# Kernel optimization log

Measured on AMD Instinct MI355X. Metric: run time of the kernel, lower is better.

Reference implementation:

```python
import jax, jax.numpy as jnp
import numpy as np

B, C, T, K = 64, 12, 2048, 2048
LMAX = 11            # max kernel length among {7,9,11}
CMAX = C - 1         # torch.randint(1, C) -> at most C-1 selected channels
PL = 1024            # left pad: covers max 'same' left pad = (dil*(len-1))//2 <= (T-1)//2
PR = 3412            # right pad: covers zero-weight padded taps (LMAX-1)*dil_max
A = 7.0              # softppv_param


def setup_inputs() -> dict:
    rng = np.random.default_rng(0)
    klens = rng.choice(np.array([7, 9, 11]), size=K)
    nch = rng.integers(1, C, size=K)  # 1..C-1 channels per kernel
    weights = np.zeros((K, CMAX, LMAX), np.float32)
    ch_idx = np.zeros((K, CMAX), np.int32)
    dils = np.zeros(K, np.int32)
    offs = np.zeros(K, np.int32)
    olens = np.zeros(K, np.int32)
    for k in range(K):
        n, L = int(nch[k]), int(klens[k])
        ch_idx[k, :n] = rng.permutation(C)[:n]
        w = rng.standard_normal((n, L)).astype(np.float32)
        w -= w.mean(axis=1, keepdims=True)  # per-channel mean-centering as in torch init
        weights[k, :n, :L] = w
        d = int(2.0 ** rng.uniform(0.0, np.log2((T - 1) / (L - 1))))
        dils[k] = d
        if rng.integers(0, 2) == 0:  # padding='same' (torch: left=total//2, right=rest)
            offs[k] = PL - (d * (L - 1)) // 2
            olens[k] = T
        else:                        # padding='valid'
            offs[k] = PL
            olens[k] = T - d * (L - 1)
    biases = rng.uniform(0.0, 1.0, size=K).astype(np.float32)
    x = jax.random.normal(jax.random.key(0), (B, C, T), jnp.float32)
    return {
        "x": x,
        "weights": jnp.asarray(weights),
        "biases": jnp.asarray(biases),
        "ch_idx": jnp.asarray(ch_idx),
        "dils": jnp.asarray(dils),
        "offs": jnp.asarray(offs),
        "olens": jnp.asarray(olens),
    }


def reference(x, weights, biases, ch_idx, dils, offs, olens):
    # x: (B, C, T). Zero-pad time axis once so every (same/valid, dilation) variant
    # becomes a pure gather with a per-kernel offset; zero-padded weight taps/channels
    # contribute nothing, so padded gathers are harmless.
    xpad = jnp.pad(x, ((0, 0), (0, 0), (PL, PR)))
    t = jnp.arange(T)
    l = jnp.arange(LMAX)

    def step(_, p):
        W, b, ch, d, off, olen = p
        pos = off + t[:, None] + l[None, :] * d            # (T, LMAX) tap positions
        Xg = xpad[:, ch, :][:, :, pos]                     # (B, CMAX, T, LMAX)
        y = jnp.einsum('bctl,cl->bt', Xg, W) + b           # cross-correlation + bias
        mask = t < olen                                    # valid output positions
        ppv = jnp.sum(jax.nn.sigmoid(A * y - 3.0) * mask, axis=-1) / olen
        mx = jnp.max(jnp.where(mask, y, -jnp.inf), axis=-1)
        return None, (ppv, mx)

    _, (ppvs, mxs) = jax.lax.scan(step, None, (weights, biases, ch_idx, dils, offs, olens))
    # torch concatenates [ppv_k, max_k] per kernel along the feature axis -> (B, 2K)
    return jnp.stack([ppvs.T, mxs.T], axis=-1).reshape(x.shape[0], 2 * K)
```

## Files before the change

kernel.cpp:

```cpp
#include <hip/hip_runtime.h>
#include <math.h>

#define B_SZ   64
#define C_SZ   12
#define T_SZ   2048
#define K_SZ   2048
#define LMAX   11
#define CMAX   11
#define NPAIR  6
#define PL_PAD 1024
#define A_PARAM 7.0f

#define NW     8
#define BLOCK_MAIN (NW * 64)
#define R      16
#define SPL    4
#define NBLK   768

typedef _Float16 h2 __attribute__((ext_vector_type(2)));

__device__ __forceinline__ float fdot2f(unsigned w, unsigned v, float acc) {
    return __builtin_amdgcn_fdot2(__builtin_bit_cast(h2, w),
                                  __builtin_bit_cast(h2, v), acc, false);
}

__global__ __launch_bounds__(256) void trh_kernel(const float* __restrict__ x,
                                                  unsigned short* __restrict__ xT) {
    const int c    = blockIdx.x;
    const int lane = threadIdx.x & 63;
    const int wid  = threadIdx.x >> 6;
    const int t0   = blockIdx.y * 128 + wid * 32;
    const float* xrow = x + ((size_t)lane * C_SZ + c) * T_SZ + t0;
    unsigned short* dst = xT + ((size_t)c * T_SZ + t0) * 64 + lane;
    #pragma unroll 8
    for (int i = 0; i < 32; ++i) {
        const _Float16 h = (_Float16)xrow[i];
        dst[i * 64] = __builtin_bit_cast(unsigned short, h);
    }
}

__global__ __launch_bounds__(1024) void sched_kernel(const float* __restrict__ w,
                                                     const int* __restrict__ olens,
                                                     unsigned* __restrict__ perm,
                                                     unsigned* __restrict__ meta,
                                                     unsigned* __restrict__ counter) {
    __shared__ unsigned key[K_SZ];
    const int tid = threadIdx.x;
    if (tid == 0) *counter = 0u;

    for (int k = tid; k < K_SZ; k += 1024) {
        const float* wk = w + (size_t)k * (CMAX * LMAX);
        int n = 0, L = 0;
        for (int e = 0; e < CMAX * LMAX; ++e) {
            if (wk[e] != 0.0f) {
                const int c = e / LMAX, l = e % LMAX;
                n = max(n, c + 1);
                L = max(L, l + 1);
            }
        }
        meta[k] = (unsigned)n | ((unsigned)L << 8);
        const unsigned cost = (unsigned)(n * L) * (unsigned)((olens[k] + 127) >> 7);
        key[k] = (cost << 11) | (unsigned)k;
    }
    __syncthreads();

    for (int ksz = 2; ksz <= K_SZ; ksz <<= 1) {
        for (int j = ksz >> 1; j > 0; j >>= 1) {
            for (int i = tid; i < K_SZ; i += 1024) {
                const int ixj = i ^ j;
                if (ixj > i) {
                    const unsigned a = key[i], b = key[ixj];
                    const bool sw = ((i & ksz) == 0) ? (a < b) : (a > b);
                    if (sw) { key[i] = b; key[ixj] = a; }
                }
            }
            __syncthreads();
        }
    }
    for (int i = tid; i < K_SZ; i += 1024)
        perm[i] = key[i] & 0x7FFu;
}

template<int LC>
__device__ __forceinline__ void conv_all(
    const unsigned short* __restrict__ xT,
    const int*      __restrict__ sCh,
    const unsigned  (* __restrict__ sWp)[LMAX],
    int npair, int d, int offr, int olen, float bias, int sp,
    int lane, int wid, float& psum, float& pmax)
{
    constexpr int NV = R + LC - 1;

    const int nj   = (olen + d - 1) / d;
    const int njb  = (nj + R - 1) / R;
    const int S    = (d >= 64) ? 1 : ((64 + d - 1) / d);
    const int len  = (njb + S - 1) / S;
    const int nunits = d * S;

    for (int u = sp * NW + wid; u < nunits; u += NW * SPL) {
        int q, seg;
        if (S == 1) { q = u; seg = 0; }
        else        { q = u % d; seg = u / d; }
        const int jb0 = seg * len;
        const int jb1 = min(njb, jb0 + len);

        for (int jb = jb0; jb < jb1; ++jb) {
            const int tq = q + jb * (R * d);
            if (tq >= olen) break;
            const int tpos0 = tq + offr;

            float y[R];
            #pragma unroll
            for (int r = 0; r < R; ++r) y[r] = bias;

            const bool fast = (tpos0 >= 0) && (tpos0 + (NV - 1) * d < T_SZ);

            if (fast) {
                for (int p = 0; p < npair; ++p) {
                    const int rbA = __builtin_amdgcn_readfirstlane(sCh[2*p  ] * T_SZ + tpos0);
                    const int rbB = __builtin_amdgcn_readfirstlane(sCh[2*p+1] * T_SZ + tpos0);
                    const unsigned short* rpA = xT + ((size_t)rbA << 6);
                    const unsigned short* rpB = xT + ((size_t)rbB << 6);

                    unsigned vp[NV];
                    #pragma unroll
                    for (int i = 0; i < NV; ++i) {
                        const unsigned a = rpA[lane];
                        const unsigned b = rpB[lane];
                        vp[i] = __builtin_amdgcn_perm(b, a, 0x05040100);
                        rpA += (d << 6); rpB += (d << 6);
                    }

                    const unsigned* wrow = &sWp[p][0];
                    #pragma unroll
                    for (int l = 0; l < LC; ++l) {
                        const unsigned w = wrow[l];
                        #pragma unroll
                        for (int r = 0; r < R; ++r)
                            y[r] = fdot2f(w, vp[l + r], y[r]);
                    }
                }
            } else {
                for (int p = 0; p < npair; ++p) {
                    const int rbA = __builtin_amdgcn_readfirstlane(sCh[2*p  ] * T_SZ);
                    const int rbB = __builtin_amdgcn_readfirstlane(sCh[2*p+1] * T_SZ);
                    const unsigned short* rowA = xT + ((size_t)rbA << 6);
                    const unsigned short* rowB = xT + ((size_t)rbB << 6);

                    unsigned vp[NV];
                    #pragma unroll
                    for (int i = 0; i < NV; ++i) {
                        const int tp  = tpos0 + i * d;
                        const int tpc = min(max(tp, 0), T_SZ - 1);
                        const unsigned a = rowA[((size_t)tpc << 6) + lane];
                        const unsigned b = rowB[((size_t)tpc << 6) + lane];
                        const unsigned pk = __builtin_amdgcn_perm(b, a, 0x05040100);
                        vp[i] = ((unsigned)tp < (unsigned)T_SZ) ? pk : 0u;
                    }

                    const unsigned* wrow = &sWp[p][0];
                    #pragma unroll
                    for (int l = 0; l < LC; ++l) {
                        const unsigned w = wrow[l];
                        #pragma unroll
                        for (int r = 0; r < R; ++r)
                            y[r] = fdot2f(w, vp[l + r], y[r]);
                    }
                }
            }

            #pragma unroll
            for (int r = 0; r < R; ++r) {
                const int t = tq + r * d;
                if (t < olen) {
                    psum += 1.0f / (1.0f + __expf(3.0f - A_PARAM * y[r]));
                    pmax  = fmaxf(pmax, y[r]);
                }
            }
        }
    }
}

__global__ __launch_bounds__(BLOCK_MAIN, 3) void rocket_tr(
    const unsigned short* __restrict__ xT,
    const unsigned* __restrict__ perm,
    const unsigned* __restrict__ meta,
    const float* __restrict__ weights,
    const float* __restrict__ biases,
    const int*   __restrict__ ch_idx,
    const int*   __restrict__ dils,
    const int*   __restrict__ offs,
    const int*   __restrict__ olens,
    float*       __restrict__ part,
    unsigned*    __restrict__ counter)
{
    __shared__ unsigned sWp[NPAIR][LMAX];
    __shared__ int      sCh[2 * NPAIR];
    __shared__ int      sItem;
    __shared__ float    sP[NW][64];
    __shared__ float    sM[NW][64];

    const int tid  = threadIdx.x;
    const int lane = tid & 63;
    const int wid  = __builtin_amdgcn_readfirstlane(tid >> 6);

    for (;;) {
        __syncthreads();
        if (tid == 0) sItem = (int)atomicAdd(counter, 1u);
        __syncthreads();
        const int item = sItem;
        if (item >= K_SZ * SPL) break;

        const int kidx = item / SPL;
        const int sp   = item % SPL;
        const int k    = (int)perm[kidx];

        if (tid < NPAIR * LMAX) {
            const int p = tid / LMAX;
            const int l = tid % LMAX;
            const float wA = weights[(size_t)k * (CMAX * LMAX) + (2 * p) * LMAX + l];
            const float wB = (2 * p + 1 < CMAX)
                ? weights[(size_t)k * (CMAX * LMAX) + (2 * p + 1) * LMAX + l] : 0.0f;
            h2 hh; hh.x = (_Float16)wA; hh.y = (_Float16)wB;
            sWp[p][l] = __builtin_bit_cast(unsigned, hh);
        }
        if (tid >= 64 && tid < 64 + 2 * NPAIR) {
            const int c = tid - 64;
            sCh[c] = (c < CMAX) ? ch_idx[(size_t)k * CMAX + c] : 0;
        }
        __syncthreads();

        const unsigned mk = meta[k];
        const int   n     = (int)(mk & 0xFFu);
        const int   L     = (int)((mk >> 8) & 0xFFu);
        const int   npair = (n + 1) >> 1;
        const int   d     = dils[k];
        const int   offr  = offs[k] - PL_PAD;
        const int   olen  = olens[k];
        const float bias  = biases[k];

        float psum = 0.0f;
        float pmax = -INFINITY;

        if (L <= 7)
            conv_all<7 >(xT, sCh, sWp, npair, d, offr, olen, bias, sp, lane, wid, psum, pmax);
        else if (L <= 9)
            conv_all<9 >(xT, sCh, sWp, npair, d, offr, olen, bias, sp, lane, wid, psum, pmax);
        else
            conv_all<11>(xT, sCh, sWp, npair, d, offr, olen, bias, sp, lane, wid, psum, pmax);

        sP[wid][lane] = psum;
        sM[wid][lane] = pmax;
        __syncthreads();

        if (tid < 64) {
            float s = 0.0f, m = -INFINITY;
            #pragma unroll
            for (int w = 0; w < NW; ++w) {
                s += sP[w][tid];
                m  = fmaxf(m, sM[w][tid]);
            }
            float* pp = part + ((size_t)k * SPL + sp) * 128;
            pp[tid]      = s;
            pp[64 + tid] = m;
        }
    }
}

__global__ __launch_bounds__(256) void combine_kernel(
    const float* __restrict__ part,
    const int*   __restrict__ olens,
    float*       __restrict__ out)
{
    const int idx = blockIdx.x * 256 + threadIdx.x;
    if (idx >= K_SZ * 64) return;
    const int k = idx >> 6;
    const int b = idx & 63;
    const float* pp = part + (size_t)k * SPL * 128;
    float s = 0.0f, m = -INFINITY;
    #pragma unroll
    for (int sp = 0; sp < SPL; ++sp) {
        s += pp[sp * 128 + b];
        m  = fmaxf(m, pp[sp * 128 + 64 + b]);
    }
    out[(size_t)b * (2 * K_SZ) + 2 * k]     = s / (float)olens[k];
    out[(size_t)b * (2 * K_SZ) + 2 * k + 1] = m;
}

__global__ __launch_bounds__(256) void rocket_fallback(
    const float* __restrict__ x,
    const float* __restrict__ weights,
    const float* __restrict__ biases,
    const int*   __restrict__ ch_idx,
    const int*   __restrict__ dils,
    const int*   __restrict__ offs,
    const int*   __restrict__ olens,
    float*       __restrict__ out)
{
    __shared__ float sW[CMAX][LMAX];
    __shared__ int   sCh[CMAX];
    __shared__ float sRed[2][4];

    const int k   = blockIdx.x;
    const int tid = threadIdx.x;

    if (tid < CMAX * LMAX)
        sW[tid / LMAX][tid % LMAX] = weights[(size_t)k * (CMAX * LMAX) + tid];
    if (tid < CMAX)
        sCh[tid] = ch_idx[(size_t)k * CMAX + tid];
    __syncthreads();

    const int   d    = dils[k];
    const int   off  = offs[k] - PL_PAD;
    const int   olen = olens[k];
    const float bias = biases[k];
    const int   lane = tid & 63;
    const int   wid  = tid >> 6;

    for (int b = blockIdx.y; b < B_SZ; b += gridDim.y) {
        float psum = 0.0f, pmax = -INFINITY;
        for (int t = tid; t < T_SZ; t += 256) {
            float y = bias;
            for (int c = 0; c < CMAX; ++c) {
                const float* xb = x + ((size_t)b * C_SZ + sCh[c]) * T_SZ;
                int pos = off + t;
                for (int l = 0; l < LMAX; ++l) {
                    const float xv = ((unsigned)pos < (unsigned)T_SZ) ? xb[pos] : 0.0f;
                    y = fmaf(sW[c][l], xv, y);
                    pos += d;
                }
            }
            if (t < olen) {
                psum += 1.0f / (1.0f + __expf(3.0f - A_PARAM * y));
                pmax = fmaxf(pmax, y);
            }
        }
        for (int o = 32; o > 0; o >>= 1) {
            psum += __shfl_down(psum, o, 64);
            pmax  = fmaxf(pmax, __shfl_down(pmax, o, 64));
        }
        if (lane == 0) { sRed[0][wid] = psum; sRed[1][wid] = pmax; }
        __syncthreads();
        if (tid == 0) {
            const float s = sRed[0][0] + sRed[0][1] + sRed[0][2] + sRed[0][3];
            const float m = fmaxf(fmaxf(sRed[1][0], sRed[1][1]),
                                  fmaxf(sRed[1][2], sRed[1][3]));
            out[(size_t)b * (2 * K_SZ) + 2 * k]     = s / (float)olen;
            out[(size_t)b * (2 * K_SZ) + 2 * k + 1] = m;
        }
        __syncthreads();
    }
}

extern "C" void kernel_launch(void* const* d_in, const int* in_sizes, int n_in,
                              void* d_out, int out_size, void* d_ws, size_t ws_size,
                              hipStream_t stream) {
    const float* x       = (const float*)d_in[0];
    const float* weights = (const float*)d_in[1];
    const float* biases  = (const float*)d_in[2];
    const int*   ch_idx  = (const int*)  d_in[3];
    const int*   dils    = (const int*)  d_in[4];
    const int*   offs    = (const int*)  d_in[5];
    const int*   olens   = (const int*)  d_in[6];
    float*       out     = (float*)d_out;

    const size_t xt_bytes   = (size_t)C_SZ * T_SZ * 64 * sizeof(unsigned short);
    const size_t perm_bytes = K_SZ * sizeof(unsigned);
    const size_t meta_bytes = K_SZ * sizeof(unsigned);
    const size_t part_bytes = (size_t)K_SZ * SPL * 128 * sizeof(float);
    const size_t need       = xt_bytes + perm_bytes + meta_bytes + part_bytes + 128;

    if (ws_size >= need) {
        char* wsb = (char*)d_ws;
        unsigned short* xT   = (unsigned short*)wsb;
        unsigned* perm       = (unsigned*)(wsb + xt_bytes);
        unsigned* meta       = (unsigned*)(wsb + xt_bytes + perm_bytes);
        float*    part       = (float*)(wsb + xt_bytes + perm_bytes + meta_bytes);
        unsigned* counter    = (unsigned*)(wsb + xt_bytes + perm_bytes + meta_bytes + part_bytes);

        dim3 tgrid(C_SZ, T_SZ / 128);
        trh_kernel<<<tgrid, 256, 0, stream>>>(x, xT);
        sched_kernel<<<1, 1024, 0, stream>>>(weights, olens, perm, meta, counter);
        rocket_tr<<<NBLK, BLOCK_MAIN, 0, stream>>>(xT, perm, meta, weights,
                                                   biases, ch_idx, dils, offs,
                                                   olens, part, counter);
        combine_kernel<<<(K_SZ * 64 + 255) / 256, 256, 0, stream>>>(part, olens, out);
    } else {
        dim3 grid(K_SZ, 16);
        rocket_fallback<<<grid, 256, 0, stream>>>(x, weights, biases, ch_idx,
                                                  dils, offs, olens, out);
    }
}
```

Baseline: 638.2 us.

## Double-buffer channel-pair loads in conv fast path and halve output tile

Halves the per-thread output tile R from 16 to 8. The fast path now software-pipelines the channel-pair loop with two register buffers, so the loads for the next pair are issued before the fdot2 math on the current pair. Packing two halves now uses a vector-of-u16 bitcast in place of v_perm. The aim is to hide global load latency behind compute; the cost is more register pressure from the double buffer, offset by the smaller R, and less tap reuse per load.

```diff
diff --git a/kernel.cpp b/kernel.cpp
--- a/kernel.cpp
+++ b/kernel.cpp
@@ -13,11 +13,12 @@
 
 #define NW     8
 #define BLOCK_MAIN (NW * 64)
-#define R      16
+#define R      8
 #define SPL    4
 #define NBLK   768
 
 typedef _Float16 h2 __attribute__((ext_vector_type(2)));
+typedef unsigned short u16x2 __attribute__((ext_vector_type(2)));
 
 __device__ __forceinline__ float fdot2f(unsigned w, unsigned v, float acc) {
     return __builtin_amdgcn_fdot2(__builtin_bit_cast(h2, w),
@@ -81,6 +82,32 @@
         perm[i] = key[i] & 0x7FFu;
 }
 
+#define LOADP(P, VP) do {                                                      \
+    const int rbA_ = __builtin_amdgcn_readfirstlane(sCh[2*(P)  ] * T_SZ + tpos0); \
+    const int rbB_ = __builtin_amdgcn_readfirstlane(sCh[2*(P)+1] * T_SZ + tpos0); \
+    const unsigned short* rpA_ = xT + ((size_t)rbA_ << 6);                     \
+    const unsigned short* rpB_ = xT + ((size_t)rbB_ << 6);                     \
+    _Pragma("unroll")                                                          \
+    for (int i_ = 0; i_ < NV; ++i_) {                                          \
+        u16x2 v_;                                                              \
+        v_.x = rpA_[lane];                                                     \
+        v_.y = rpB_[lane];                                                     \
+        VP[i_] = __builtin_bit_cast(unsigned, v_);                             \
+        rpA_ += (d << 6); rpB_ += (d << 6);                                    \
+    }                                                                          \
+} while (0)
+
+#define FMAP(P, VP) do {                                                       \
+    const unsigned* wrow_ = &sWp[(P)][0];                                      \
+    _Pragma("unroll")                                                          \
+    for (int l_ = 0; l_ < LC; ++l_) {                                          \
+        const unsigned wl_ = wrow_[l_];                                        \
+        _Pragma("unroll")                                                      \
+        for (int r_ = 0; r_ < R; ++r_)                                         \
+            y[r_] = fdot2f(wl_, VP[l_ + r_], y[r_]);                           \
+    }                                                                          \
+} while (0)
+
 template<int LC>
 __device__ __forceinline__ void conv_all(
     const unsigned short* __restrict__ xT,
@@ -116,29 +143,16 @@
             const bool fast = (tpos0 >= 0) && (tpos0 + (NV - 1) * d < T_SZ);
 
             if (fast) {
-                for (int p = 0; p < npair; ++p) {
-                    const int rbA = __builtin_amdgcn_readfirstlane(sCh[2*p  ] * T_SZ + tpos0);
-                    const int rbB = __builtin_amdgcn_readfirstlane(sCh[2*p+1] * T_SZ + tpos0);
-                    const unsigned short* rpA = xT + ((size_t)rbA << 6);
-                    const unsigned short* rpB = xT + ((size_t)rbB << 6);
-
-                    unsigned vp[NV];
-                    #pragma unroll
-                    for (int i = 0; i < NV; ++i) {
-                        const unsigned a = rpA[lane];
-                        const unsigned b = rpB[lane];
-                        vp[i] = __builtin_amdgcn_perm(b, a, 0x05040100);
-                        rpA += (d << 6); rpB += (d << 6);
-                    }
-
-                    const unsigned* wrow = &sWp[p][0];
-                    #pragma unroll
-                    for (int l = 0; l < LC; ++l) {
-                        const unsigned w = wrow[l];
-                        #pragma unroll
-                        for (int r = 0; r < R; ++r)
-                            y[r] = fdot2f(w, vp[l + r], y[r]);
-                    }
+                unsigned vpA[NV], vpB[NV];
+                LOADP(0, vpA);
+                int p = 0;
+                for (;;) {
+                    if (p + 1 < npair) LOADP(p + 1, vpB);
+                    FMAP(p, vpA);
+                    if (++p >= npair) break;
+                    if (p + 1 < npair) LOADP(p + 1, vpA);
+                    FMAP(p, vpB);
+                    if (++p >= npair) break;
                 }
             } else {
                 for (int p = 0; p < npair; ++p) {
```

After: 644.2 us. Within noise of the previous version (+0.9%).
